# Kernel optimization log

Measured on AMD Instinct MI355X. Metric: run time of the kernel, lower is better.

## Reference

```python
import jax, jax.numpy as jnp
import numpy as np

B, T, C = 4, 4096, 256

def setup_inputs() -> dict:
    key = jax.random.key(0)
    kx, km, kk, kq, kv = jax.random.split(key, 5)
    x = jax.random.normal(kx, (B, T, C), dtype=jnp.float32)
    mask = jax.random.randint(km, (B, T), 0, 2, dtype=jnp.int32)
    s = C ** -0.5
    Wk = jax.random.normal(kk, (C, C), dtype=jnp.float32) * s
    Wq = jax.random.normal(kq, (C, C), dtype=jnp.float32) * s
    Wv = jax.random.normal(kv, (C, C), dtype=jnp.float32) * s
    return {"x": x, "mask": mask, "Wk": Wk, "Wq": Wq, "Wv": Wv}

def reference(x, mask, Wk, Wq, Wv):
    # nn.Linear: y = x @ W.T  (W is [out, in])
    k = jnp.einsum('btc,dc->btd', x, Wk)   # [B,T,C]
    q = jnp.einsum('btc,dc->btd', x, Wq)   # [B,T,C]
    v = jnp.einsum('btc,dc->btd', x, Wv)   # [B,T,C]
    scale = k.shape[-1] ** -0.5
    weights = jnp.einsum('bqc,bkc->bqk', q, k) * scale  # [B,T,T]
    # torch quirk: mask.float().masked_fill(mask==0, -inf) adds +1.0 where mask!=0
    mask_f = jnp.where(mask == 0, -jnp.inf, mask.astype(weights.dtype))  # [B,T]
    masked = weights + mask_f[:, None, :]   # broadcast over query dim == repeat(1,T,1)
    attn = jax.nn.softmax(masked, axis=-1)
    out = jnp.einsum('bqk,bkc->bqc', attn, v)  # [B,T,C]
    return out
```

## Files before the change

### kernel.cpp

```cpp
#include <hip/hip_runtime.h>


typedef __attribute__((ext_vector_type(8)))  _Float16 f16x8;
typedef __attribute__((ext_vector_type(4)))  _Float16 f16x4;
typedef __attribute__((ext_vector_type(4)))  float    f32x4;
typedef __attribute__((ext_vector_type(16))) float    f32x16;

constexpr int Bb = 4;
constexpr int Tt = 4096;
constexpr int Cc = 256;
constexpr int BT = Bb * Tt;

#define MFMA16(a, b, c) __builtin_amdgcn_mfma_f32_16x16x32_f16((a), (b), (c), 0, 0, 0)
#define MFMA32(a, b, c) __builtin_amdgcn_mfma_f32_32x32x16_f16((a), (b), (c), 0, 0, 0)

__global__ __launch_bounds__(256) void qkv_proj(
    const float* __restrict__ x,
    const float* __restrict__ Wq, const float* __restrict__ Wk,
    const float* __restrict__ Wv,
    _Float16* __restrict__ qo, _Float16* __restrict__ ko,
    _Float16* __restrict__ vto)
{
    extern __shared__ _Float16 sm[];
    _Float16* xs = sm;
    _Float16* wsm = sm + 128 * 264;

    const int tid = threadIdx.x;
    const int m0  = blockIdx.x * 128;
    const int ny  = blockIdx.y;
    const int mat = ny >> 1;
    const int d0  = (ny & 1) * 128;
    const float* W = (mat == 0) ? Wq : (mat == 1 ? Wk : Wv);

#pragma unroll
    for (int i = 0; i < 32; ++i) {
        int flat = i * 256 + tid;
        int r = flat >> 6, c4 = (flat & 63) << 2;
        float4 v = *reinterpret_cast<const float4*>(x + (size_t)(m0 + r) * Cc + c4);
        f16x4 h = { (_Float16)v.x, (_Float16)v.y, (_Float16)v.z, (_Float16)v.w };
        *reinterpret_cast<f16x4*>(xs + r * 264 + c4) = h;
    }
#pragma unroll
    for (int i = 0; i < 32; ++i) {
        int flat = i * 256 + tid;
        int r = flat >> 6, c4 = (flat & 63) << 2;
        float4 v = *reinterpret_cast<const float4*>(W + (size_t)(d0 + r) * Cc + c4);
        f16x4 h = { (_Float16)v.x, (_Float16)v.y, (_Float16)v.z, (_Float16)v.w };
        *reinterpret_cast<f16x4*>(wsm + r * 264 + c4) = h;
    }
    __syncthreads();

    const int w = tid >> 6, lane = tid & 63;
    const int lr = lane & 15, lg = lane >> 4;

    f32x4 acc[2][8] = {};

#pragma unroll
    for (int kc = 0; kc < 8; ++kc) {
        const int c0 = kc * 32 + lg * 8;
        f16x8 xf[2], wf[8];
#pragma unroll
        for (int mb = 0; mb < 2; ++mb)
            xf[mb] = *reinterpret_cast<const f16x8*>(xs + (w * 32 + mb * 16 + lr) * 264 + c0);
#pragma unroll
        for (int db = 0; db < 8; ++db)
            wf[db] = *reinterpret_cast<const f16x8*>(wsm + (db * 16 + lr) * 264 + c0);
        if (mat != 2) {
#pragma unroll
            for (int mb = 0; mb < 2; ++mb)
#pragma unroll
                for (int db = 0; db < 8; ++db)
                    acc[mb][db] = MFMA16(wf[db], xf[mb], acc[mb][db]);
        } else {
#pragma unroll
            for (int mb = 0; mb < 2; ++mb)
#pragma unroll
                for (int db = 0; db < 8; ++db)
                    acc[mb][db] = MFMA16(xf[mb], wf[db], acc[mb][db]);
        }
    }

    if (mat != 2) {
        const float sc = (mat == 0) ? 0.0625f : 1.0f;
        const int jj  = (lg & 1) * 4;
#pragma unroll
        for (int mb = 0; mb < 2; ++mb)
#pragma unroll
            for (int db = 0; db < 8; ++db) {
                int m  = m0 + w * 32 + mb * 16 + lr;
                int c  = d0 + db * 16 + lg * 4;
                int kc = c >> 5;
                int ch = (c >> 3) & 3;
                f32x4 a = acc[mb][db];
                f16x4 h = { (_Float16)(a.x * sc), (_Float16)(a.y * sc),
                            (_Float16)(a.z * sc), (_Float16)(a.w * sc) };
                if (mat == 0) {
                    size_t off = (size_t)(m >> 5) * 8192 + (((m >> 4) & 1) * 8 + kc) * 512
                               + ch * 128 + (m & 15) * 8 + jj;
                    *reinterpret_cast<f16x4*>(qo + off) = h;
                } else {
                    size_t off = (size_t)(m >> 4) * 4096 + kc * 512
                               + ch * 128 + (m & 15) * 8 + jj;
                    *reinterpret_cast<f16x4*>(ko + off) = h;
                }
            }
    } else {
        const int jj = (lg & 1) * 4;
        const int kh = (lg >> 1) & 1;
#pragma unroll
        for (int mb = 0; mb < 2; ++mb)
#pragma unroll
            for (int db = 0; db < 8; ++db) {
                int d = d0 + db * 16 + lr;
                int m = m0 + w * 32 + mb * 16 + lg * 4;
                f32x4 a = acc[mb][db];
                f16x4 h = { (_Float16)a.x, (_Float16)a.y, (_Float16)a.z, (_Float16)a.w };
                size_t off = (size_t)(m >> 4) * 4096 + (d >> 5) * 512
                           + kh * 256 + (d & 31) * 8 + jj;
                *reinterpret_cast<f16x4*>(vto + off) = h;
            }
    }
}

__global__ __launch_bounds__(256, 1) void attn_kernel(
    const _Float16* __restrict__ qb, const _Float16* __restrict__ kb,
    const _Float16* __restrict__ vtb, const int* __restrict__ mask,
    float* __restrict__ outp)
{
    extern __shared__ char smraw[];
    float* mex  = (float*)(smraw + 6144);
    float* lex  = (float*)(smraw + 6656);
    float* oexf = (float*)(smraw + 8192);

    const int tid = threadIdx.x, w = tid >> 6, lane = tid & 63;
    const int qw = w >> 1, g = w & 1;
    const int l15 = lane & 15, l4 = lane >> 4;
    const int l31 = lane & 31, l5 = lane >> 5;

    const int bid = blockIdx.x;
    const int b   = (bid & 7) >> 1;
    const int qt  = ((bid >> 3) << 1) | (bid & 1);
    const int q0  = qt * 64;
    const size_t base = (size_t)b * Tt * Cc;
    const int* maskb = mask + (size_t)b * Tt;
    const _Float16* kTb = kb + base;
    const _Float16* vTb = vtb + base;

    f16x8 qf[2][8];
    {
        const _Float16* qTb = qb + (size_t)(b * 128 + qt * 2 + qw) * 8192;
#pragma unroll
        for (int qh = 0; qh < 2; ++qh)
#pragma unroll
            for (int kc = 0; kc < 8; ++kc)
                qf[qh][kc] = *reinterpret_cast<const f16x8*>(
                    qTb + (qh * 8 + kc) * 512 + l4 * 128 + l15 * 8);
    }

    _Float16* pw = (_Float16*)smraw + w * 768;

    f32x16 o[8] = {};
    float m0r = -60.f, m1r = -60.f, l0r = 0.f, l1r = 0.f;

    auto LOADT = [&](f16x8 (&kr)[8], f16x8 (&vr)[8], int4& mc, int tile) {
        const _Float16* kp = kTb + (size_t)tile * 4096 + l4 * 128 + l15 * 8;
#pragma unroll
        for (int kc = 0; kc < 8; ++kc)
            kr[kc] = *reinterpret_cast<const f16x8*>(kp + kc * 512);
        const _Float16* vp = vTb + (size_t)tile * 4096 + l5 * 256 + l31 * 8;
#pragma unroll
        for (int dt = 0; dt < 8; ++dt)
            vr[dt] = *reinterpret_cast<const f16x8*>(vp + dt * 512);
        mc = *reinterpret_cast<const int4*>(maskb + tile * 16 + l4 * 4);
    };

    auto COMPUTE = [&](f16x8 (&kr)[8], f16x8 (&vr)[8], int4 mc) {
        f32x4 s40 = { 0.f, 0.f, 0.f, 0.f }, s41 = { 0.f, 0.f, 0.f, 0.f };
#pragma unroll
        for (int kc = 0; kc < 8; ++kc) {
            s40 = MFMA16(kr[kc], qf[0][kc], s40);
            s41 = MFMA16(kr[kc], qf[1][kc], s41);
        }
        if (mc.x == 0) { s40[0] = -1e30f; s41[0] = -1e30f; }
        if (mc.y == 0) { s40[1] = -1e30f; s41[1] = -1e30f; }
        if (mc.z == 0) { s40[2] = -1e30f; s41[2] = -1e30f; }
        if (mc.w == 0) { s40[3] = -1e30f; s41[3] = -1e30f; }

        float t0 = fmaxf(fmaxf(s40[0], s40[1]), fmaxf(s40[2], s40[3]));
        float t1 = fmaxf(fmaxf(s41[0], s41[1]), fmaxf(s41[2], s41[3]));
        t0 = fmaxf(t0, __shfl_xor(t0, 16, 64)); t0 = fmaxf(t0, __shfl_xor(t0, 32, 64));
        t1 = fmaxf(t1, __shfl_xor(t1, 16, 64)); t1 = fmaxf(t1, __shfl_xor(t1, 32, 64));

        if (__any(t0 > m0r + 8.f || t1 > m1r + 8.f)) {
            float mn0 = fmaxf(m0r, t0), mn1 = fmaxf(m1r, t1);
            float c0 = __expf(m0r - mn0), c1 = __expf(m1r - mn1);
            m0r = mn0; m1r = mn1; l0r *= c0; l1r *= c1;
            float cs = (lane & 16) ? c1 : c0;
#pragma unroll
            for (int dt = 0; dt < 8; ++dt) o[dt] *= cs;
        }

        float rs0 = 0.f, rs1 = 0.f;
#pragma unroll
        for (int r = 0; r < 4; ++r) {
            float p0 = __expf(s40[r] - m0r); s40[r] = p0; rs0 += p0;
            float p1 = __expf(s41[r] - m1r); s41[r] = p1; rs1 += p1;
        }
        rs0 += __shfl_xor(rs0, 16, 64); rs0 += __shfl_xor(rs0, 32, 64);
        rs1 += __shfl_xor(rs1, 16, 64); rs1 += __shfl_xor(rs1, 32, 64);
        l0r += rs0; l1r += rs1;

        {
            f16x4 h0 = { (_Float16)s40[0], (_Float16)s40[1], (_Float16)s40[2], (_Float16)s40[3] };
            f16x4 h1 = { (_Float16)s41[0], (_Float16)s41[1], (_Float16)s41[2], (_Float16)s41[3] };
            *reinterpret_cast<f16x4*>(pw + l15 * 24 + l4 * 4)        = h0;
            *reinterpret_cast<f16x4*>(pw + (16 + l15) * 24 + l4 * 4) = h1;
        }
        f16x8 pf = *reinterpret_cast<const f16x8*>(pw + l31 * 24 + l5 * 8);

#pragma unroll
        for (int dt = 0; dt < 8; ++dt)
            o[dt] = MFMA32(vr[dt], pf, o[dt]);
    };

    f16x8 kA[8], vA[8], kB[8], vB[8];
    int4 mA_, mB_;
    const int ktb = g * 128;
    LOADT(kA, vA, mA_, ktb);
#pragma unroll 1
    for (int t2 = 0; t2 < 64; ++t2) {
        LOADT(kB, vB, mB_, ktb + 2 * t2 + 1);
        COMPUTE(kA, vA, mA_);
        LOADT(kA, vA, mA_, (2 * t2 + 2 < 128) ? (ktb + 2 * t2 + 2) : ktb);
        COMPUTE(kB, vB, mB_);
    }

    __syncthreads();
    if (l4 == 0) {
        mex[w * 32 + l15]      = m0r;  mex[w * 32 + 16 + l15] = m1r;
        lex[w * 32 + l15]      = l0r;  lex[w * 32 + 16 + l15] = l1r;
    }
    __syncthreads();

    {
        float mq  = (lane & 16) ? m1r : m0r;
        float mA2 = mex[(qw * 2 + 0) * 32 + l31];
        float mB2 = mex[(qw * 2 + 1) * 32 + l31];
        float mst = fmaxf(mA2, mB2);
        float osc = __expf(mq - mst);
        float* oq = oexf + qw * (32 * 258);
        if (g == 1) {
#pragma unroll
            for (int dt = 0; dt < 8; ++dt)
#pragma unroll
                for (int r = 0; r < 16; ++r) {
                    int d = dt * 32 + (r & 3) + 8 * (r >> 2) + 4 * l5;
                    oq[l31 * 258 + d] = o[dt][r] * osc;
                }
        }
        __syncthreads();
        if (g == 0) {
#pragma unroll
            for (int dt = 0; dt < 8; ++dt)
#pragma unroll
                for (int r = 0; r < 16; ++r) {
                    int d = dt * 32 + (r & 3) + 8 * (r >> 2) + 4 * l5;
                    oq[l31 * 258 + d] += o[dt][r] * osc;
                }
        }
        __syncthreads();
    }

    {
        const int q = tid >> 2, ds0 = (tid & 3) * 64;
        const int qws = q >> 5, ql = q & 31;
        float mA2 = mex[(qws * 2 + 0) * 32 + ql];
        float mB2 = mex[(qws * 2 + 1) * 32 + ql];
        float ms  = fmaxf(mA2, mB2);
        float lt  = lex[(qws * 2 + 0) * 32 + ql] * __expf(mA2 - ms)
                  + lex[(qws * 2 + 1) * 32 + ql] * __expf(mB2 - ms);
        float inv = 1.f / lt;
        const float* src = oexf + qws * (32 * 258) + ql * 258 + ds0;
        float* dst = outp + base + (size_t)(q0 + q) * Cc + ds0;
#pragma unroll
        for (int i = 0; i < 16; ++i) {
            f32x4 a = *reinterpret_cast<const f32x4*>(src + 4 * i);
            a[0] *= inv; a[1] *= inv; a[2] *= inv; a[3] *= inv;
            *reinterpret_cast<f32x4*>(dst + 4 * i) = a;
        }
    }
}

extern "C" void kernel_launch(void* const* d_in, const int* in_sizes, int n_in,
                              void* d_out, int out_size, void* d_ws, size_t ws_size,
                              hipStream_t stream)
{
    (void)in_sizes; (void)n_in; (void)out_size; (void)ws_size;
    const float* x   = (const float*)d_in[0];
    const int*  mask = (const int*)d_in[1];
    const float* Wk  = (const float*)d_in[2];
    const float* Wq  = (const float*)d_in[3];
    const float* Wv  = (const float*)d_in[4];
    float* out = (float*)d_out;

    _Float16* q  = (_Float16*)d_ws;
    _Float16* k  = q + (size_t)BT * Cc;
    _Float16* vt = k + (size_t)BT * Cc;

    dim3 gA(128, 6), blkA(256);
    size_t ldsA = (size_t)(128 + 128) * 264 * sizeof(_Float16);
    qkv_proj<<<gA, blkA, ldsA, stream>>>(x, Wq, Wk, Wv, q, k, vt);

    dim3 gB(256), blkB(256);
    size_t ldsB = 74240;
    attn_kernel<<<gB, blkB, ldsB, stream>>>(q, k, vt, mask, out);
}
```

Before: 128.5 us.

## Switch attention QK to 32x32 MFMA tiles with 32-key steps and additive mask bias

Each wave's score block now comes from 32x32x16 MFMAs over 32-key tiles instead of 16x16x32 MFMAs over 16-key tiles. Q, K and V^T are stored in a new 32-row blocked layout to match. A separate kernel turns the int mask into an additive float bias so the attention loop adds it instead of branching. Softmax reductions drop to one cross-half shuffle and loop iterations halve. The cost is an extra launch, more workspace, and heavier register pressure from 16-entry K/V fragment arrays with single buffering.

```diff
diff --git a/kernel.cpp b/kernel.cpp
--- a/kernel.cpp
+++ b/kernel.cpp
@@ -10,9 +10,16 @@
 constexpr int Tt = 4096;
 constexpr int Cc = 256;
 constexpr int BT = Bb * Tt;
+constexpr int NT = 64;
 
 #define MFMA16(a, b, c) __builtin_amdgcn_mfma_f32_16x16x32_f16((a), (b), (c), 0, 0, 0)
 #define MFMA32(a, b, c) __builtin_amdgcn_mfma_f32_32x32x16_f16((a), (b), (c), 0, 0, 0)
+
+__global__ __launch_bounds__(256) void mask_prep(const int* __restrict__ m,
+                                                 float* __restrict__ mf) {
+    int i = blockIdx.x * 256 + threadIdx.x;
+    mf[i] = (m[i] == 0) ? -1e30f : 0.0f;
+}
 
 __global__ __launch_bounds__(256) void qkv_proj(
     const float* __restrict__ x,
@@ -82,31 +89,22 @@
 
     if (mat != 2) {
         const float sc = (mat == 0) ? 0.0625f : 1.0f;
-        const int jj  = (lg & 1) * 4;
+        _Float16* dst = (mat == 0) ? qo : ko;
 #pragma unroll
         for (int mb = 0; mb < 2; ++mb)
 #pragma unroll
             for (int db = 0; db < 8; ++db) {
                 int m  = m0 + w * 32 + mb * 16 + lr;
                 int c  = d0 + db * 16 + lg * 4;
-                int kc = c >> 5;
-                int ch = (c >> 3) & 3;
+                int s  = c >> 4, h2 = (c >> 3) & 1, j0 = c & 7;
                 f32x4 a = acc[mb][db];
                 f16x4 h = { (_Float16)(a.x * sc), (_Float16)(a.y * sc),
                             (_Float16)(a.z * sc), (_Float16)(a.w * sc) };
-                if (mat == 0) {
-                    size_t off = (size_t)(m >> 5) * 8192 + (((m >> 4) & 1) * 8 + kc) * 512
-                               + ch * 128 + (m & 15) * 8 + jj;
-                    *reinterpret_cast<f16x4*>(qo + off) = h;
-                } else {
-                    size_t off = (size_t)(m >> 4) * 4096 + kc * 512
-                               + ch * 128 + (m & 15) * 8 + jj;
-                    *reinterpret_cast<f16x4*>(ko + off) = h;
-                }
+                size_t off = (size_t)(m >> 5) * 8192 + s * 512 + h2 * 256
+                           + (m & 31) * 8 + j0;
+                *reinterpret_cast<f16x4*>(dst + off) = h;
             }
     } else {
-        const int jj = (lg & 1) * 4;
-        const int kh = (lg >> 1) & 1;
 #pragma unroll
         for (int mb = 0; mb < 2; ++mb)
 #pragma unroll
@@ -115,8 +113,9 @@
                 int m = m0 + w * 32 + mb * 16 + lg * 4;
                 f32x4 a = acc[mb][db];
                 f16x4 h = { (_Float16)a.x, (_Float16)a.y, (_Float16)a.z, (_Float16)a.w };
-                size_t off = (size_t)(m >> 4) * 4096 + (d >> 5) * 512
-                           + kh * 256 + (d & 31) * 8 + jj;
+                size_t off = (size_t)(m >> 5) * 8192 + (size_t)(d >> 5) * 1024
+                           + ((m >> 4) & 1) * 512 + ((m >> 3) & 1) * 256
+                           + (d & 31) * 8 + (m & 7);
                 *reinterpret_cast<f16x4*>(vto + off) = h;
             }
     }
@@ -124,137 +123,145 @@
 
 __global__ __launch_bounds__(256, 1) void attn_kernel(
     const _Float16* __restrict__ qb, const _Float16* __restrict__ kb,
-    const _Float16* __restrict__ vtb, const int* __restrict__ mask,
+    const _Float16* __restrict__ vtb, const float* __restrict__ maskf,
     float* __restrict__ outp)
 {
     extern __shared__ char smraw[];
-    float* mex  = (float*)(smraw + 6144);
-    float* lex  = (float*)(smraw + 6656);
-    float* oexf = (float*)(smraw + 8192);
+    float* mex  = (float*)(smraw);
+    float* lex  = (float*)(smraw + 512);
+    float* oexf = (float*)(smraw + 10240);
 
     const int tid = threadIdx.x, w = tid >> 6, lane = tid & 63;
     const int qw = w >> 1, g = w & 1;
-    const int l15 = lane & 15, l4 = lane >> 4;
-    const int l31 = lane & 31, l5 = lane >> 5;
+    const int l31 = lane & 31, h = lane >> 5;
 
     const int bid = blockIdx.x;
     const int b   = (bid & 7) >> 1;
     const int qt  = ((bid >> 3) << 1) | (bid & 1);
     const int q0  = qt * 64;
     const size_t base = (size_t)b * Tt * Cc;
-    const int* maskb = mask + (size_t)b * Tt;
     const _Float16* kTb = kb + base;
     const _Float16* vTb = vtb + base;
-
-    f16x8 qf[2][8];
+    const float* mfb = maskf + (size_t)b * Tt;
+
+    f16x8 qf[16];
     {
-        const _Float16* qTb = qb + (size_t)(b * 128 + qt * 2 + qw) * 8192;
-#pragma unroll
-        for (int qh = 0; qh < 2; ++qh)
-#pragma unroll
-            for (int kc = 0; kc < 8; ++kc)
-                qf[qh][kc] = *reinterpret_cast<const f16x8*>(
-                    qTb + (qh * 8 + kc) * 512 + l4 * 128 + l15 * 8);
-    }
-
-    _Float16* pw = (_Float16*)smraw + w * 768;
+        const _Float16* qTb = qb + (size_t)(b * 128 + qt * 2 + qw) * 8192
+                            + h * 256 + l31 * 8;
+#pragma unroll
+        for (int s = 0; s < 16; ++s)
+            qf[s] = *reinterpret_cast<const f16x8*>(qTb + s * 512);
+    }
+
+    _Float16* pw = (_Float16*)(smraw + 1024) + w * (32 * 36);
 
     f32x16 o[8] = {};
-    float m0r = -60.f, m1r = -60.f, l0r = 0.f, l1r = 0.f;
-
-    auto LOADT = [&](f16x8 (&kr)[8], f16x8 (&vr)[8], int4& mc, int tile) {
-        const _Float16* kp = kTb + (size_t)tile * 4096 + l4 * 128 + l15 * 8;
-#pragma unroll
-        for (int kc = 0; kc < 8; ++kc)
-            kr[kc] = *reinterpret_cast<const f16x8*>(kp + kc * 512);
-        const _Float16* vp = vTb + (size_t)tile * 4096 + l5 * 256 + l31 * 8;
-#pragma unroll
-        for (int dt = 0; dt < 8; ++dt)
-            vr[dt] = *reinterpret_cast<const f16x8*>(vp + dt * 512);
-        mc = *reinterpret_cast<const int4*>(maskb + tile * 16 + l4 * 4);
+    float m_run = -60.f, l_run = 0.f;
+
+    f16x8 kr[16], vr[16];
+    f32x4 bb[4];
+
+    const int tb = g * 64;
+
+    auto LOADK = [&](int t) {
+        const _Float16* p = kTb + (size_t)t * 8192 + h * 256 + l31 * 8;
+#pragma unroll
+        for (int s = 0; s < 16; ++s)
+            kr[s] = *reinterpret_cast<const f16x8*>(p + s * 512);
     };
-
-    auto COMPUTE = [&](f16x8 (&kr)[8], f16x8 (&vr)[8], int4 mc) {
-        f32x4 s40 = { 0.f, 0.f, 0.f, 0.f }, s41 = { 0.f, 0.f, 0.f, 0.f };
-#pragma unroll
-        for (int kc = 0; kc < 8; ++kc) {
-            s40 = MFMA16(kr[kc], qf[0][kc], s40);
-            s41 = MFMA16(kr[kc], qf[1][kc], s41);
-        }
-        if (mc.x == 0) { s40[0] = -1e30f; s41[0] = -1e30f; }
-        if (mc.y == 0) { s40[1] = -1e30f; s41[1] = -1e30f; }
-        if (mc.z == 0) { s40[2] = -1e30f; s41[2] = -1e30f; }
-        if (mc.w == 0) { s40[3] = -1e30f; s41[3] = -1e30f; }
-
-        float t0 = fmaxf(fmaxf(s40[0], s40[1]), fmaxf(s40[2], s40[3]));
-        float t1 = fmaxf(fmaxf(s41[0], s41[1]), fmaxf(s41[2], s41[3]));
-        t0 = fmaxf(t0, __shfl_xor(t0, 16, 64)); t0 = fmaxf(t0, __shfl_xor(t0, 32, 64));
-        t1 = fmaxf(t1, __shfl_xor(t1, 16, 64)); t1 = fmaxf(t1, __shfl_xor(t1, 32, 64));
-
-        if (__any(t0 > m0r + 8.f || t1 > m1r + 8.f)) {
-            float mn0 = fmaxf(m0r, t0), mn1 = fmaxf(m1r, t1);
-            float c0 = __expf(m0r - mn0), c1 = __expf(m1r - mn1);
-            m0r = mn0; m1r = mn1; l0r *= c0; l1r *= c1;
-            float cs = (lane & 16) ? c1 : c0;
+    auto LOADV = [&](int t) {
+        const _Float16* p = vTb + (size_t)t * 8192 + h * 256 + l31 * 8;
+#pragma unroll
+        for (int i = 0; i < 16; ++i)
+            vr[i] = *reinterpret_cast<const f16x8*>(p + i * 512);
+    };
+    auto LOADB = [&](int t) {
+        const float* p = mfb + t * 32 + 4 * h;
+#pragma unroll
+        for (int gg = 0; gg < 4; ++gg)
+            bb[gg] = *reinterpret_cast<const f32x4*>(p + gg * 8);
+    };
+
+    LOADK(tb); LOADV(tb); LOADB(tb);
+
+#pragma unroll 1
+    for (int t = 0; t < NT; ++t) {
+        const int tn = (t + 1 < NT) ? (tb + t + 1) : tb;
+
+        f32x16 sA = {}, sB = {};
+#pragma unroll
+        for (int s = 0; s < 8; ++s) {
+            sA = MFMA32(kr[2 * s],     qf[2 * s],     sA);
+            sB = MFMA32(kr[2 * s + 1], qf[2 * s + 1], sB);
+        }
+        LOADK(tn);
+
+        float S[16];
+#pragma unroll
+        for (int r = 0; r < 16; ++r)
+            S[r] = sA[r] + sB[r] + bb[r >> 2][r & 3];
+        LOADB(tn);
+
+        float a0 = fmaxf(S[0], S[1]),   a1 = fmaxf(S[2], S[3]);
+        float a2 = fmaxf(S[4], S[5]),   a3 = fmaxf(S[6], S[7]);
+        float a4 = fmaxf(S[8], S[9]),   a5 = fmaxf(S[10], S[11]);
+        float a6 = fmaxf(S[12], S[13]), a7 = fmaxf(S[14], S[15]);
+        float tm = fmaxf(fmaxf(fmaxf(a0, a1), fmaxf(a2, a3)),
+                         fmaxf(fmaxf(a4, a5), fmaxf(a6, a7)));
+        tm = fmaxf(tm, __shfl_xor(tm, 32, 64));
+
+        if (__any(tm > m_run + 8.f)) {
+            float mn = fmaxf(m_run, tm);
+            float cs = __expf(m_run - mn);
+            m_run = mn; l_run *= cs;
 #pragma unroll
             for (int dt = 0; dt < 8; ++dt) o[dt] *= cs;
         }
 
-        float rs0 = 0.f, rs1 = 0.f;
-#pragma unroll
-        for (int r = 0; r < 4; ++r) {
-            float p0 = __expf(s40[r] - m0r); s40[r] = p0; rs0 += p0;
-            float p1 = __expf(s41[r] - m1r); s41[r] = p1; rs1 += p1;
-        }
-        rs0 += __shfl_xor(rs0, 16, 64); rs0 += __shfl_xor(rs0, 32, 64);
-        rs1 += __shfl_xor(rs1, 16, 64); rs1 += __shfl_xor(rs1, 32, 64);
-        l0r += rs0; l1r += rs1;
-
-        {
-            f16x4 h0 = { (_Float16)s40[0], (_Float16)s40[1], (_Float16)s40[2], (_Float16)s40[3] };
-            f16x4 h1 = { (_Float16)s41[0], (_Float16)s41[1], (_Float16)s41[2], (_Float16)s41[3] };
-            *reinterpret_cast<f16x4*>(pw + l15 * 24 + l4 * 4)        = h0;
-            *reinterpret_cast<f16x4*>(pw + (16 + l15) * 24 + l4 * 4) = h1;
-        }
-        f16x8 pf = *reinterpret_cast<const f16x8*>(pw + l31 * 24 + l5 * 8);
-
-#pragma unroll
-        for (int dt = 0; dt < 8; ++dt)
-            o[dt] = MFMA32(vr[dt], pf, o[dt]);
-    };
-
-    f16x8 kA[8], vA[8], kB[8], vB[8];
-    int4 mA_, mB_;
-    const int ktb = g * 128;
-    LOADT(kA, vA, mA_, ktb);
-#pragma unroll 1
-    for (int t2 = 0; t2 < 64; ++t2) {
-        LOADT(kB, vB, mB_, ktb + 2 * t2 + 1);
-        COMPUTE(kA, vA, mA_);
-        LOADT(kA, vA, mA_, (2 * t2 + 2 < 128) ? (ktb + 2 * t2 + 2) : ktb);
-        COMPUTE(kB, vB, mB_);
+        float p[16];
+#pragma unroll
+        for (int r = 0; r < 16; ++r) p[r] = __expf(S[r] - m_run);
+        float s0 = (p[0] + p[1]) + (p[2] + p[3]);
+        float s1 = (p[4] + p[5]) + (p[6] + p[7]);
+        float s2 = (p[8] + p[9]) + (p[10] + p[11]);
+        float s3 = (p[12] + p[13]) + (p[14] + p[15]);
+        float rs = (s0 + s1) + (s2 + s3);
+        rs += __shfl_xor(rs, 32, 64);
+        l_run += rs;
+
+#pragma unroll
+        for (int gg = 0; gg < 4; ++gg) {
+            f16x4 hh = { (_Float16)p[4 * gg], (_Float16)p[4 * gg + 1],
+                         (_Float16)p[4 * gg + 2], (_Float16)p[4 * gg + 3] };
+            *reinterpret_cast<f16x4*>(pw + l31 * 36 + gg * 8 + 4 * h) = hh;
+        }
+        f16x8 pf0 = *reinterpret_cast<const f16x8*>(pw + l31 * 36 + h * 8);
+        f16x8 pf1 = *reinterpret_cast<const f16x8*>(pw + l31 * 36 + 16 + h * 8);
+
+#pragma unroll
+        for (int dt = 0; dt < 8; ++dt) {
+            o[dt] = MFMA32(vr[2 * dt],     pf0, o[dt]);
+            o[dt] = MFMA32(vr[2 * dt + 1], pf1, o[dt]);
+        }
+        LOADV(tn);
     }
 
     __syncthreads();
-    if (l4 == 0) {
-        mex[w * 32 + l15]      = m0r;  mex[w * 32 + 16 + l15] = m1r;
-        lex[w * 32 + l15]      = l0r;  lex[w * 32 + 16 + l15] = l1r;
-    }
+    if (h == 0) { mex[w * 32 + l31] = m_run; lex[w * 32 + l31] = l_run; }
     __syncthreads();
 
     {
-        float mq  = (lane & 16) ? m1r : m0r;
         float mA2 = mex[(qw * 2 + 0) * 32 + l31];
         float mB2 = mex[(qw * 2 + 1) * 32 + l31];
         float mst = fmaxf(mA2, mB2);
-        float osc = __expf(mq - mst);
+        float osc = __expf(m_run - mst);
         float* oq = oexf + qw * (32 * 258);
         if (g == 1) {
 #pragma unroll
             for (int dt = 0; dt < 8; ++dt)
 #pragma unroll
                 for (int r = 0; r < 16; ++r) {
-                    int d = dt * 32 + (r & 3) + 8 * (r >> 2) + 4 * l5;
+                    int d = dt * 32 + (r & 3) + 8 * (r >> 2) + 4 * h;
                     oq[l31 * 258 + d] = o[dt][r] * osc;
                 }
         }
@@ -264,7 +271,7 @@
             for (int dt = 0; dt < 8; ++dt)
 #pragma unroll
                 for (int r = 0; r < 16; ++r) {
-                    int d = dt * 32 + (r & 3) + 8 * (r >> 2) + 4 * l5;
+                    int d = dt * 32 + (r & 3) + 8 * (r >> 2) + 4 * h;
                     oq[l31 * 258 + d] += o[dt][r] * osc;
                 }
         }
@@ -306,12 +313,15 @@
     _Float16* q  = (_Float16*)d_ws;
     _Float16* k  = q + (size_t)BT * Cc;
     _Float16* vt = k + (size_t)BT * Cc;
+    float* maskf = (float*)(vt + (size_t)BT * Cc);
+
+    mask_prep<<<BT / 256, 256, 0, stream>>>(mask, maskf);
 
     dim3 gA(128, 6), blkA(256);
     size_t ldsA = (size_t)(128 + 128) * 264 * sizeof(_Float16);
     qkv_proj<<<gA, blkA, ldsA, stream>>>(x, Wq, Wk, Wv, q, k, vt);
 
     dim3 gB(256), blkB(256);
-    size_t ldsB = 74240;
-    attn_kernel<<<gB, blkB, ldsB, stream>>>(q, k, vt, mask, out);
+    size_t ldsB = 76288;
+    attn_kernel<<<gB, blkB, ldsB, stream>>>(q, k, vt, maskf, out);
 }
```

Result: slower. 158.3 us (+23.2%).

## Process two key tiles per softmax step and restructure K/V prefetch pipeline

Applied to the files above, without the earlier changes.

The attention inner loop now computes QK scores for two 16-key tiles before running a single online-softmax update. That halves the max/sum shuffles, the rescale checks and the LDS round-trips for P per pair of tiles. K loads for the next tiles are issued right after each QK, and V loads after the PV MFMAs, so the prefetch is split by operand. The P staging buffer grows to hold 32 keys per row, and the LDS offsets and size change to match. The cost is more live registers and a longer dependency chain per iteration, which could hurt latency hiding.

```diff
diff --git a/kernel.cpp b/kernel.cpp
--- a/kernel.cpp
+++ b/kernel.cpp
@@ -128,9 +128,9 @@
     float* __restrict__ outp)
 {
     extern __shared__ char smraw[];
-    float* mex  = (float*)(smraw + 6144);
-    float* lex  = (float*)(smraw + 6656);
-    float* oexf = (float*)(smraw + 8192);
+    float* mex  = (float*)(smraw + 10240);
+    float* lex  = (float*)(smraw + 10752);
+    float* oexf = (float*)(smraw + 11264);
 
     const int tid = threadIdx.x, w = tid >> 6, lane = tid & 63;
     const int qw = w >> 1, g = w & 1;
@@ -157,37 +157,63 @@
                     qTb + (qh * 8 + kc) * 512 + l4 * 128 + l15 * 8);
     }
 
-    _Float16* pw = (_Float16*)smraw + w * 768;
+    _Float16* pw = (_Float16*)smraw + w * 1280;
 
     f32x16 o[8] = {};
     float m0r = -60.f, m1r = -60.f, l0r = 0.f, l1r = 0.f;
 
-    auto LOADT = [&](f16x8 (&kr)[8], f16x8 (&vr)[8], int4& mc, int tile) {
+    auto LOADK = [&](f16x8 (&kr)[8], int tile) {
         const _Float16* kp = kTb + (size_t)tile * 4096 + l4 * 128 + l15 * 8;
 #pragma unroll
         for (int kc = 0; kc < 8; ++kc)
             kr[kc] = *reinterpret_cast<const f16x8*>(kp + kc * 512);
+    };
+    auto LOADV = [&](f16x8 (&vr)[8], int tile) {
         const _Float16* vp = vTb + (size_t)tile * 4096 + l5 * 256 + l31 * 8;
 #pragma unroll
         for (int dt = 0; dt < 8; ++dt)
             vr[dt] = *reinterpret_cast<const f16x8*>(vp + dt * 512);
-        mc = *reinterpret_cast<const int4*>(maskb + tile * 16 + l4 * 4);
     };
 
-    auto COMPUTE = [&](f16x8 (&kr)[8], f16x8 (&vr)[8], int4 mc) {
-        f32x4 s40 = { 0.f, 0.f, 0.f, 0.f }, s41 = { 0.f, 0.f, 0.f, 0.f };
+    auto QK = [&](f16x8 (&kr)[8], int4 mc, f32x4& s0, f32x4& s1) {
+        s0 = (f32x4){ 0.f, 0.f, 0.f, 0.f };
+        s1 = (f32x4){ 0.f, 0.f, 0.f, 0.f };
 #pragma unroll
         for (int kc = 0; kc < 8; ++kc) {
-            s40 = MFMA16(kr[kc], qf[0][kc], s40);
-            s41 = MFMA16(kr[kc], qf[1][kc], s41);
-        }
-        if (mc.x == 0) { s40[0] = -1e30f; s41[0] = -1e30f; }
-        if (mc.y == 0) { s40[1] = -1e30f; s41[1] = -1e30f; }
-        if (mc.z == 0) { s40[2] = -1e30f; s41[2] = -1e30f; }
-        if (mc.w == 0) { s40[3] = -1e30f; s41[3] = -1e30f; }
-
-        float t0 = fmaxf(fmaxf(s40[0], s40[1]), fmaxf(s40[2], s40[3]));
-        float t1 = fmaxf(fmaxf(s41[0], s41[1]), fmaxf(s41[2], s41[3]));
+            s0 = MFMA16(kr[kc], qf[0][kc], s0);
+            s1 = MFMA16(kr[kc], qf[1][kc], s1);
+        }
+        if (mc.x == 0) { s0[0] = -1e30f; s1[0] = -1e30f; }
+        if (mc.y == 0) { s0[1] = -1e30f; s1[1] = -1e30f; }
+        if (mc.z == 0) { s0[2] = -1e30f; s1[2] = -1e30f; }
+        if (mc.w == 0) { s0[3] = -1e30f; s1[3] = -1e30f; }
+    };
+
+    f16x8 kA[8], kB[8], vA[8], vB[8];
+    int4 mA_, mB_;
+    const int ktb = g * 128;
+    LOADK(kA, ktb);     LOADK(kB, ktb + 1);
+    LOADV(vA, ktb);     LOADV(vB, ktb + 1);
+    mA_ = *reinterpret_cast<const int4*>(maskb + ktb * 16 + l4 * 4);
+    mB_ = *reinterpret_cast<const int4*>(maskb + (ktb + 1) * 16 + l4 * 4);
+
+#pragma unroll 1
+    for (int t2 = 0; t2 < 64; ++t2) {
+        const int tnA = (t2 < 63) ? (ktb + 2 * t2 + 2) : ktb;
+        const int tnB = (t2 < 63) ? (ktb + 2 * t2 + 3) : ktb;
+
+        f32x4 sa0, sa1, sb0, sb1;
+        QK(kA, mA_, sa0, sa1);
+        LOADK(kA, tnA);
+        QK(kB, mB_, sb0, sb1);
+        LOADK(kB, tnB);
+        int4 mA2 = *reinterpret_cast<const int4*>(maskb + tnA * 16 + l4 * 4);
+        int4 mB2 = *reinterpret_cast<const int4*>(maskb + tnB * 16 + l4 * 4);
+
+        float t0 = fmaxf(fmaxf(fmaxf(sa0[0], sa0[1]), fmaxf(sa0[2], sa0[3])),
+                         fmaxf(fmaxf(sb0[0], sb0[1]), fmaxf(sb0[2], sb0[3])));
+        float t1 = fmaxf(fmaxf(fmaxf(sa1[0], sa1[1]), fmaxf(sa1[2], sa1[3])),
+                         fmaxf(fmaxf(sb1[0], sb1[1]), fmaxf(sb1[2], sb1[3])));
         t0 = fmaxf(t0, __shfl_xor(t0, 16, 64)); t0 = fmaxf(t0, __shfl_xor(t0, 32, 64));
         t1 = fmaxf(t1, __shfl_xor(t1, 16, 64)); t1 = fmaxf(t1, __shfl_xor(t1, 32, 64));
 
@@ -203,36 +229,38 @@
         float rs0 = 0.f, rs1 = 0.f;
 #pragma unroll
         for (int r = 0; r < 4; ++r) {
-            float p0 = __expf(s40[r] - m0r); s40[r] = p0; rs0 += p0;
-            float p1 = __expf(s41[r] - m1r); s41[r] = p1; rs1 += p1;
+            float p;
+            p = __expf(sa0[r] - m0r); sa0[r] = p; rs0 += p;
+            p = __expf(sb0[r] - m0r); sb0[r] = p; rs0 += p;
+            p = __expf(sa1[r] - m1r); sa1[r] = p; rs1 += p;
+            p = __expf(sb1[r] - m1r); sb1[r] = p; rs1 += p;
         }
         rs0 += __shfl_xor(rs0, 16, 64); rs0 += __shfl_xor(rs0, 32, 64);
         rs1 += __shfl_xor(rs1, 16, 64); rs1 += __shfl_xor(rs1, 32, 64);
         l0r += rs0; l1r += rs1;
 
         {
-            f16x4 h0 = { (_Float16)s40[0], (_Float16)s40[1], (_Float16)s40[2], (_Float16)s40[3] };
-            f16x4 h1 = { (_Float16)s41[0], (_Float16)s41[1], (_Float16)s41[2], (_Float16)s41[3] };
-            *reinterpret_cast<f16x4*>(pw + l15 * 24 + l4 * 4)        = h0;
-            *reinterpret_cast<f16x4*>(pw + (16 + l15) * 24 + l4 * 4) = h1;
-        }
-        f16x8 pf = *reinterpret_cast<const f16x8*>(pw + l31 * 24 + l5 * 8);
-
-#pragma unroll
-        for (int dt = 0; dt < 8; ++dt)
-            o[dt] = MFMA32(vr[dt], pf, o[dt]);
-    };
-
-    f16x8 kA[8], vA[8], kB[8], vB[8];
-    int4 mA_, mB_;
-    const int ktb = g * 128;
-    LOADT(kA, vA, mA_, ktb);
-#pragma unroll 1
-    for (int t2 = 0; t2 < 64; ++t2) {
-        LOADT(kB, vB, mB_, ktb + 2 * t2 + 1);
-        COMPUTE(kA, vA, mA_);
-        LOADT(kA, vA, mA_, (2 * t2 + 2 < 128) ? (ktb + 2 * t2 + 2) : ktb);
-        COMPUTE(kB, vB, mB_);
+            f16x4 h;
+            h = (f16x4){ (_Float16)sa0[0], (_Float16)sa0[1], (_Float16)sa0[2], (_Float16)sa0[3] };
+            *reinterpret_cast<f16x4*>(pw + l15 * 40 + l4 * 4) = h;
+            h = (f16x4){ (_Float16)sb0[0], (_Float16)sb0[1], (_Float16)sb0[2], (_Float16)sb0[3] };
+            *reinterpret_cast<f16x4*>(pw + l15 * 40 + 16 + l4 * 4) = h;
+            h = (f16x4){ (_Float16)sa1[0], (_Float16)sa1[1], (_Float16)sa1[2], (_Float16)sa1[3] };
+            *reinterpret_cast<f16x4*>(pw + (16 + l15) * 40 + l4 * 4) = h;
+            h = (f16x4){ (_Float16)sb1[0], (_Float16)sb1[1], (_Float16)sb1[2], (_Float16)sb1[3] };
+            *reinterpret_cast<f16x4*>(pw + (16 + l15) * 40 + 16 + l4 * 4) = h;
+        }
+        f16x8 pf0 = *reinterpret_cast<const f16x8*>(pw + l31 * 40 + l5 * 8);
+        f16x8 pf1 = *reinterpret_cast<const f16x8*>(pw + l31 * 40 + 16 + l5 * 8);
+
+#pragma unroll
+        for (int dt = 0; dt < 8; ++dt) {
+            o[dt] = MFMA32(vA[dt], pf0, o[dt]);
+            o[dt] = MFMA32(vB[dt], pf1, o[dt]);
+        }
+        LOADV(vA, tnA);
+        LOADV(vB, tnB);
+        mA_ = mA2; mB_ = mB2;
     }
 
     __syncthreads();
@@ -312,6 +340,6 @@
     qkv_proj<<<gA, blkA, ldsA, stream>>>(x, Wq, Wk, Wv, q, k, vt);
 
     dim3 gB(256), blkB(256);
-    size_t ldsB = 74240;
+    size_t ldsB = 77312;
     attn_kernel<<<gB, blkB, ldsB, stream>>>(q, k, vt, mask, out);
 }
```

New measurement: 129.5 us. About the same (+0.8%).

## Restructure attention kernel: 32-query tiles, LDS-staged K via async loads, 2 blocks/CU

Applied to the files above, without the earlier changes.

The attention kernel now processes 32 queries per block (512 blocks, launch bounds 2 per CU) instead of 64. K tiles are staged into a 4-deep LDS ring with global_load_lds, and V is read in 32-key groups using 16x16 MFMAs. The V layout written by the projection kernel changes to match. Softmax updates are batched over two key tiles and MFMA sections get raised scheduling priority. The aim is more occupancy and better latency hiding, at the cost of a barrier every iteration and more LDS traffic per K tile.

```diff
diff --git a/kernel.cpp b/kernel.cpp
--- a/kernel.cpp
+++ b/kernel.cpp
@@ -4,7 +4,6 @@
 typedef __attribute__((ext_vector_type(8)))  _Float16 f16x8;
 typedef __attribute__((ext_vector_type(4)))  _Float16 f16x4;
 typedef __attribute__((ext_vector_type(4)))  float    f32x4;
-typedef __attribute__((ext_vector_type(16))) float    f32x16;
 
 constexpr int Bb = 4;
 constexpr int Tt = 4096;
@@ -12,7 +11,12 @@
 constexpr int BT = Bb * Tt;
 
 #define MFMA16(a, b, c) __builtin_amdgcn_mfma_f32_16x16x32_f16((a), (b), (c), 0, 0, 0)
-#define MFMA32(a, b, c) __builtin_amdgcn_mfma_f32_32x32x16_f16((a), (b), (c), 0, 0, 0)
+
+__device__ __forceinline__ void gl16(const _Float16* gp, char* lp) {
+    __builtin_amdgcn_global_load_lds(
+        (const __attribute__((address_space(1))) void*)gp,
+        (__attribute__((address_space(3))) void*)lp, 16, 0, 0);
+}
 
 __global__ __launch_bounds__(256) void qkv_proj(
     const float* __restrict__ x,
@@ -105,8 +109,6 @@
                 }
             }
     } else {
-        const int jj = (lg & 1) * 4;
-        const int kh = (lg >> 1) & 1;
 #pragma unroll
         for (int mb = 0; mb < 2; ++mb)
 #pragma unroll
@@ -115,175 +117,179 @@
                 int m = m0 + w * 32 + mb * 16 + lg * 4;
                 f32x4 a = acc[mb][db];
                 f16x4 h = { (_Float16)a.x, (_Float16)a.y, (_Float16)a.z, (_Float16)a.w };
-                size_t off = (size_t)(m >> 4) * 4096 + (d >> 5) * 512
-                           + kh * 256 + (d & 31) * 8 + jj;
+                size_t off = (size_t)(m >> 5) * 8192 + (size_t)(d >> 4) * 512
+                           + ((m & 31) >> 3) * 128 + (d & 15) * 8 + (m & 7);
                 *reinterpret_cast<f16x4*>(vto + off) = h;
             }
     }
 }
 
-__global__ __launch_bounds__(256, 1) void attn_kernel(
+__global__ __launch_bounds__(256, 2) void attn_kernel(
     const _Float16* __restrict__ qb, const _Float16* __restrict__ kb,
     const _Float16* __restrict__ vtb, const int* __restrict__ mask,
     float* __restrict__ outp)
 {
     extern __shared__ char smraw[];
-    float* mex  = (float*)(smraw + 6144);
-    float* lex  = (float*)(smraw + 6656);
-    float* oexf = (float*)(smraw + 8192);
+    float* mex  = (float*)(smraw + 70656);
+    float* lex  = (float*)(smraw + 70912);
+    float* oexf = (float*)smraw;
 
     const int tid = threadIdx.x, w = tid >> 6, lane = tid & 63;
     const int qw = w >> 1, g = w & 1;
     const int l15 = lane & 15, l4 = lane >> 4;
-    const int l31 = lane & 31, l5 = lane >> 5;
 
     const int bid = blockIdx.x;
     const int b   = (bid & 7) >> 1;
     const int qt  = ((bid >> 3) << 1) | (bid & 1);
-    const int q0  = qt * 64;
+    const int q0  = qt * 32;
     const size_t base = (size_t)b * Tt * Cc;
     const int* maskb = mask + (size_t)b * Tt;
     const _Float16* kTb = kb + base;
     const _Float16* vTb = vtb + base;
 
-    f16x8 qf[2][8];
+    f16x8 qf[8];
     {
-        const _Float16* qTb = qb + (size_t)(b * 128 + qt * 2 + qw) * 8192;
-#pragma unroll
-        for (int qh = 0; qh < 2; ++qh)
-#pragma unroll
-            for (int kc = 0; kc < 8; ++kc)
-                qf[qh][kc] = *reinterpret_cast<const f16x8*>(
-                    qTb + (qh * 8 + kc) * 512 + l4 * 128 + l15 * 8);
-    }
-
-    _Float16* pw = (_Float16*)smraw + w * 768;
-
-    f32x16 o[8] = {};
-    float m0r = -60.f, m1r = -60.f, l0r = 0.f, l1r = 0.f;
-
-    auto LOADT = [&](f16x8 (&kr)[8], f16x8 (&vr)[8], int4& mc, int tile) {
-        const _Float16* kp = kTb + (size_t)tile * 4096 + l4 * 128 + l15 * 8;
+        const _Float16* qTb = qb + (size_t)(b * 128 + qt) * 8192;
 #pragma unroll
         for (int kc = 0; kc < 8; ++kc)
-            kr[kc] = *reinterpret_cast<const f16x8*>(kp + kc * 512);
-        const _Float16* vp = vTb + (size_t)tile * 4096 + l5 * 256 + l31 * 8;
-#pragma unroll
-        for (int dt = 0; dt < 8; ++dt)
-            vr[dt] = *reinterpret_cast<const f16x8*>(vp + dt * 512);
-        mc = *reinterpret_cast<const int4*>(maskb + tile * 16 + l4 * 4);
+            qf[kc] = *reinterpret_cast<const f16x8*>(
+                qTb + (qw * 8 + kc) * 512 + l4 * 128 + l15 * 8);
+    }
+
+    _Float16* pw = (_Float16*)(smraw + 65536) + w * 640;
+    char* kslab = smraw + g * 32768;
+
+    f32x4 o[16] = {};
+    float m_run = -60.f, l_run = 0.f;
+
+    auto STAGE_K = [&](int t, int buf) {
+        char* dst = kslab + buf * 8192 + qw * 4096;
+        const _Float16* src = kTb + (size_t)(g * 128 + t) * 4096 + qw * 2048 + lane * 8;
+#pragma unroll
+        for (int j = 0; j < 4; ++j) gl16(src + j * 512, dst + j * 1024);
     };
-
-    auto COMPUTE = [&](f16x8 (&kr)[8], f16x8 (&vr)[8], int4 mc) {
-        f32x4 s40 = { 0.f, 0.f, 0.f, 0.f }, s41 = { 0.f, 0.f, 0.f, 0.f };
+    f16x8 vf[16];
+    auto LOADV = [&](int grp) {
+        const _Float16* p = vTb + (size_t)(g * 64 + grp) * 8192 + l4 * 128 + l15 * 8;
+#pragma unroll
+        for (int dt = 0; dt < 16; ++dt)
+            vf[dt] = *reinterpret_cast<const f16x8*>(p + dt * 512);
+    };
+
+    STAGE_K(0, 0);
+    STAGE_K(1, 1);
+    LOADV(0);
+
+    f32x4 sa = {}, sb = {};
+
+#pragma unroll 1
+    for (int t = 0; t < 128; ++t) {
+        __syncthreads();
+        if (t + 2 < 128) STAGE_K(t + 2, (t + 2) & 3);
+
+        const _Float16* kb_ = (const _Float16*)(kslab + (t & 3) * 8192);
+        int4 mc = *reinterpret_cast<const int4*>(maskb + (g * 128 + t) * 16 + l4 * 4);
+
+        f32x4 s = { 0.f, 0.f, 0.f, 0.f };
+        __builtin_amdgcn_s_setprio(1);
 #pragma unroll
         for (int kc = 0; kc < 8; ++kc) {
-            s40 = MFMA16(kr[kc], qf[0][kc], s40);
-            s41 = MFMA16(kr[kc], qf[1][kc], s41);
-        }
-        if (mc.x == 0) { s40[0] = -1e30f; s41[0] = -1e30f; }
-        if (mc.y == 0) { s40[1] = -1e30f; s41[1] = -1e30f; }
-        if (mc.z == 0) { s40[2] = -1e30f; s41[2] = -1e30f; }
-        if (mc.w == 0) { s40[3] = -1e30f; s41[3] = -1e30f; }
-
-        float t0 = fmaxf(fmaxf(s40[0], s40[1]), fmaxf(s40[2], s40[3]));
-        float t1 = fmaxf(fmaxf(s41[0], s41[1]), fmaxf(s41[2], s41[3]));
-        t0 = fmaxf(t0, __shfl_xor(t0, 16, 64)); t0 = fmaxf(t0, __shfl_xor(t0, 32, 64));
-        t1 = fmaxf(t1, __shfl_xor(t1, 16, 64)); t1 = fmaxf(t1, __shfl_xor(t1, 32, 64));
-
-        if (__any(t0 > m0r + 8.f || t1 > m1r + 8.f)) {
-            float mn0 = fmaxf(m0r, t0), mn1 = fmaxf(m1r, t1);
-            float c0 = __expf(m0r - mn0), c1 = __expf(m1r - mn1);
-            m0r = mn0; m1r = mn1; l0r *= c0; l1r *= c1;
-            float cs = (lane & 16) ? c1 : c0;
-#pragma unroll
-            for (int dt = 0; dt < 8; ++dt) o[dt] *= cs;
-        }
-
-        float rs0 = 0.f, rs1 = 0.f;
+            f16x8 kf = *reinterpret_cast<const f16x8*>(kb_ + kc * 512 + l4 * 128 + l15 * 8);
+            s = MFMA16(kf, qf[kc], s);
+        }
+        __builtin_amdgcn_s_setprio(0);
+
+        if (mc.x == 0) s[0] = -1e30f;
+        if (mc.y == 0) s[1] = -1e30f;
+        if (mc.z == 0) s[2] = -1e30f;
+        if (mc.w == 0) s[3] = -1e30f;
+
+        if (!(t & 1)) { sa = s; continue; }
+        sb = s;
+
+        float tl = fmaxf(fmaxf(fmaxf(sa[0], sa[1]), fmaxf(sa[2], sa[3])),
+                         fmaxf(fmaxf(sb[0], sb[1]), fmaxf(sb[2], sb[3])));
+        if (__any(tl > m_run + 8.f)) {
+            float tm = tl;
+            tm = fmaxf(tm, __shfl_xor(tm, 16, 64));
+            tm = fmaxf(tm, __shfl_xor(tm, 32, 64));
+            float mn = fmaxf(m_run, tm);
+            float cs = __expf(m_run - mn);
+            m_run = mn; l_run *= cs;
+#pragma unroll
+            for (int dt = 0; dt < 16; ++dt) o[dt] *= cs;
+        }
+
+        float rs = 0.f;
 #pragma unroll
         for (int r = 0; r < 4; ++r) {
-            float p0 = __expf(s40[r] - m0r); s40[r] = p0; rs0 += p0;
-            float p1 = __expf(s41[r] - m1r); s41[r] = p1; rs1 += p1;
-        }
-        rs0 += __shfl_xor(rs0, 16, 64); rs0 += __shfl_xor(rs0, 32, 64);
-        rs1 += __shfl_xor(rs1, 16, 64); rs1 += __shfl_xor(rs1, 32, 64);
-        l0r += rs0; l1r += rs1;
+            float p0 = __expf(sa[r] - m_run); sa[r] = p0; rs += p0;
+            float p1 = __expf(sb[r] - m_run); sb[r] = p1; rs += p1;
+        }
+        rs += __shfl_xor(rs, 16, 64);
+        rs += __shfl_xor(rs, 32, 64);
+        l_run += rs;
 
         {
-            f16x4 h0 = { (_Float16)s40[0], (_Float16)s40[1], (_Float16)s40[2], (_Float16)s40[3] };
-            f16x4 h1 = { (_Float16)s41[0], (_Float16)s41[1], (_Float16)s41[2], (_Float16)s41[3] };
-            *reinterpret_cast<f16x4*>(pw + l15 * 24 + l4 * 4)        = h0;
-            *reinterpret_cast<f16x4*>(pw + (16 + l15) * 24 + l4 * 4) = h1;
-        }
-        f16x8 pf = *reinterpret_cast<const f16x8*>(pw + l31 * 24 + l5 * 8);
-
-#pragma unroll
-        for (int dt = 0; dt < 8; ++dt)
-            o[dt] = MFMA32(vr[dt], pf, o[dt]);
-    };
-
-    f16x8 kA[8], vA[8], kB[8], vB[8];
-    int4 mA_, mB_;
-    const int ktb = g * 128;
-    LOADT(kA, vA, mA_, ktb);
-#pragma unroll 1
-    for (int t2 = 0; t2 < 64; ++t2) {
-        LOADT(kB, vB, mB_, ktb + 2 * t2 + 1);
-        COMPUTE(kA, vA, mA_);
-        LOADT(kA, vA, mA_, (2 * t2 + 2 < 128) ? (ktb + 2 * t2 + 2) : ktb);
-        COMPUTE(kB, vB, mB_);
-    }
-
+            f16x4 h0 = { (_Float16)sa[0], (_Float16)sa[1], (_Float16)sa[2], (_Float16)sa[3] };
+            f16x4 h1 = { (_Float16)sb[0], (_Float16)sb[1], (_Float16)sb[2], (_Float16)sb[3] };
+            *reinterpret_cast<f16x4*>(pw + l15 * 40 + l4 * 4)      = h0;
+            *reinterpret_cast<f16x4*>(pw + l15 * 40 + 16 + l4 * 4) = h1;
+        }
+        f16x8 pf = *reinterpret_cast<const f16x8*>(pw + l15 * 40 + l4 * 8);
+
+        __builtin_amdgcn_s_setprio(1);
+#pragma unroll
+        for (int dt = 0; dt < 16; ++dt)
+            o[dt] = MFMA16(vf[dt], pf, o[dt]);
+        __builtin_amdgcn_s_setprio(0);
+
+        if (t + 2 < 128) LOADV((t + 1) >> 1);
+    }
     __syncthreads();
-    if (l4 == 0) {
-        mex[w * 32 + l15]      = m0r;  mex[w * 32 + 16 + l15] = m1r;
-        lex[w * 32 + l15]      = l0r;  lex[w * 32 + 16 + l15] = l1r;
-    }
+
+    if (l4 == 0) { mex[w * 16 + l15] = m_run; lex[w * 16 + l15] = l_run; }
     __syncthreads();
 
     {
-        float mq  = (lane & 16) ? m1r : m0r;
-        float mA2 = mex[(qw * 2 + 0) * 32 + l31];
-        float mB2 = mex[(qw * 2 + 1) * 32 + l31];
+        float mA2 = mex[(qw * 2 + 0) * 16 + l15];
+        float mB2 = mex[(qw * 2 + 1) * 16 + l15];
         float mst = fmaxf(mA2, mB2);
-        float osc = __expf(mq - mst);
-        float* oq = oexf + qw * (32 * 258);
+        float osc = __expf(m_run - mst);
+        float* oq = oexf + (qw * 16 + l15) * 258;
         if (g == 1) {
 #pragma unroll
-            for (int dt = 0; dt < 8; ++dt)
-#pragma unroll
-                for (int r = 0; r < 16; ++r) {
-                    int d = dt * 32 + (r & 3) + 8 * (r >> 2) + 4 * l5;
-                    oq[l31 * 258 + d] = o[dt][r] * osc;
-                }
+            for (int dt = 0; dt < 16; ++dt) {
+                f32x4 v = { o[dt][0] * osc, o[dt][1] * osc, o[dt][2] * osc, o[dt][3] * osc };
+                *reinterpret_cast<f32x4*>(oq + dt * 16 + l4 * 4) = v;
+            }
         }
         __syncthreads();
         if (g == 0) {
 #pragma unroll
-            for (int dt = 0; dt < 8; ++dt)
-#pragma unroll
-                for (int r = 0; r < 16; ++r) {
-                    int d = dt * 32 + (r & 3) + 8 * (r >> 2) + 4 * l5;
-                    oq[l31 * 258 + d] += o[dt][r] * osc;
-                }
+            for (int dt = 0; dt < 16; ++dt) {
+                f32x4 v = *reinterpret_cast<const f32x4*>(oq + dt * 16 + l4 * 4);
+                v[0] += o[dt][0] * osc; v[1] += o[dt][1] * osc;
+                v[2] += o[dt][2] * osc; v[3] += o[dt][3] * osc;
+                *reinterpret_cast<f32x4*>(oq + dt * 16 + l4 * 4) = v;
+            }
         }
         __syncthreads();
     }
 
     {
-        const int q = tid >> 2, ds0 = (tid & 3) * 64;
-        const int qws = q >> 5, ql = q & 31;
-        float mA2 = mex[(qws * 2 + 0) * 32 + ql];
-        float mB2 = mex[(qws * 2 + 1) * 32 + ql];
+        const int qv = tid >> 3, ds0 = (tid & 7) * 32;
+        const int qws = qv >> 4, ql = qv & 15;
+        float mA2 = mex[(qws * 2 + 0) * 16 + ql];
+        float mB2 = mex[(qws * 2 + 1) * 16 + ql];
         float ms  = fmaxf(mA2, mB2);
-        float lt  = lex[(qws * 2 + 0) * 32 + ql] * __expf(mA2 - ms)
-                  + lex[(qws * 2 + 1) * 32 + ql] * __expf(mB2 - ms);
+        float lt  = lex[(qws * 2 + 0) * 16 + ql] * __expf(mA2 - ms)
+                  + lex[(qws * 2 + 1) * 16 + ql] * __expf(mB2 - ms);
         float inv = 1.f / lt;
-        const float* src = oexf + qws * (32 * 258) + ql * 258 + ds0;
-        float* dst = outp + base + (size_t)(q0 + q) * Cc + ds0;
-#pragma unroll
-        for (int i = 0; i < 16; ++i) {
+        const float* src = oexf + qv * 258 + ds0;
+        float* dst = outp + base + (size_t)(q0 + qv) * Cc + ds0;
+#pragma unroll
+        for (int i = 0; i < 8; ++i) {
             f32x4 a = *reinterpret_cast<const f32x4*>(src + 4 * i);
             a[0] *= inv; a[1] *= inv; a[2] *= inv; a[3] *= inv;
             *reinterpret_cast<f32x4*>(dst + 4 * i) = a;
@@ -311,7 +317,7 @@
     size_t ldsA = (size_t)(128 + 128) * 264 * sizeof(_Float16);
     qkv_proj<<<gA, blkA, ldsA, stream>>>(x, Wq, Wk, Wv, q, k, vt);
 
-    dim3 gB(256), blkB(256);
-    size_t ldsB = 74240;
+    dim3 gB(512), blkB(256);
+    size_t ldsB = 71168;
     attn_kernel<<<gB, blkB, ldsB, stream>>>(q, k, vt, mask, out);
 }
```

New measurement: 183.2 us. +42.6%, slower.
